# Performance work log

Measured on AMD Instinct MI355X. Metric: run time of the kernel, lower is better.

## Reference

```python
import jax, jax.numpy as jnp
import numpy as np

EPS = 1e-8  # torch.nn.CosineSimilarity default eps


def _one_sided_chamfer(ex, ey):
    # ex: [N, D], ey: [M, D]
    # cosine(ex_i, ey_j) = <ex_i, ey_j> / (max(||ex_i||, eps) * max(||ey_j||, eps))
    nx = jnp.maximum(jnp.linalg.norm(ex, axis=-1, keepdims=True), EPS)  # [N,1]
    ny = jnp.maximum(jnp.linalg.norm(ey, axis=-1, keepdims=True), EPS)  # [M,1]
    exn = ex / nx
    eyn = ey / ny
    sims = jnp.einsum('nd,md->nm', exn, eyn)  # [N, M] cosine matrix
    return jnp.max(sims, axis=-1)  # row-wise max -> [N]


def setup_inputs() -> dict:
    key = jax.random.key(0)
    k1, k2 = jax.random.split(key)
    ex = jax.random.normal(k1, (8192, 768), dtype=jnp.float32)
    ey = jax.random.normal(k2, (8192, 768), dtype=jnp.float32)
    return {"ex": ex, "ey": ey}


def reference(ex, ey):
    return _one_sided_chamfer(ex, ey)
```

## Files before the change

kernel.cpp:

```cpp
#include <hip/hip_runtime.h>
#include <math.h>

#define NROWS 8192
#define KDIM  768
#define BM 128
#define BN 128
#define BKB 128
#define KTILES (KDIM / BKB)
#define NBC 4
#define NBCG (NROWS / BN / NBC)

typedef int i32x4 __attribute__((ext_vector_type(4)));

static __device__ __forceinline__ unsigned enc_f(float f) {
    unsigned x = __float_as_uint(f);
    return (x & 0x80000000u) ? ~x : (x | 0x80000000u);
}
static __device__ __forceinline__ float dec_f(unsigned u) {
    unsigned x = (u & 0x80000000u) ? (u ^ 0x80000000u) : ~u;
    return __uint_as_float(x);
}

__global__ __launch_bounds__(256) void normalize_quant_k(
        const float* __restrict__ ex, const float* __restrict__ ey,
        signed char* __restrict__ q, float* __restrict__ scales,
        unsigned* __restrict__ out) {
    if (blockIdx.x < NROWS / 256)
        out[blockIdx.x * 256 + threadIdx.x] = enc_f(-INFINITY);
    const int wave = threadIdx.x >> 6, lane = threadIdx.x & 63;
    const int grow = blockIdx.x * 4 + wave;
    const float* src = (grow < NROWS) ? ex : ey;
    const int row = grow & (NROWS - 1);
    const float4* xr = (const float4*)(src + (size_t)row * KDIM);
    float4 v[3];
    #pragma unroll
    for (int g = 0; g < 3; ++g) v[g] = xr[lane + g * 64];
    float ss = 0.f, am = 0.f;
    #pragma unroll
    for (int g = 0; g < 3; ++g) {
        ss += v[g].x * v[g].x + v[g].y * v[g].y + v[g].z * v[g].z + v[g].w * v[g].w;
        am = fmaxf(am, fmaxf(fmaxf(fabsf(v[g].x), fabsf(v[g].y)),
                             fmaxf(fabsf(v[g].z), fabsf(v[g].w))));
    }
    #pragma unroll
    for (int off = 32; off > 0; off >>= 1) {
        ss += __shfl_xor(ss, off);
        am = fmaxf(am, __shfl_xor(am, off));
    }
    const float scale = 1.0f / fmaxf(sqrtf(ss), 1e-8f);
    am = fmaxf(am * scale, 1e-12f);
    if (lane == 0) scales[grow] = am * (1.0f / 127.0f);
    const float si = scale * (127.0f / am);
    int* dr = (int*)(q + (size_t)grow * KDIM);
    #pragma unroll
    for (int g = 0; g < 3; ++g) {
        int qx = min(127, max(-127, __float2int_rn(v[g].x * si)));
        int qy = min(127, max(-127, __float2int_rn(v[g].y * si)));
        int qz = min(127, max(-127, __float2int_rn(v[g].z * si)));
        int qw = min(127, max(-127, __float2int_rn(v[g].w * si)));
        dr[lane + g * 64] = (qx & 0xff) | ((qy & 0xff) << 8) |
                            ((qz & 0xff) << 16) | ((qw & 0xff) << 24);
    }
}

__global__ __launch_bounds__(256, 4) void gemm_rowmax_i8_k(
        const signed char* __restrict__ A, const signed char* __restrict__ B,
        const float* __restrict__ sa, const float* __restrict__ sb,
        unsigned* __restrict__ out) {
    __shared__ signed char As[BM * BKB];
    __shared__ signed char Bs[BN * BKB];

    const int tid  = threadIdx.x;
    const int wave = tid >> 6, lane = tid & 63;
    const int xcd = blockIdx.x & 7;
    const int idx = blockIdx.x >> 3;
    const int br  = (xcd >> 1) * 16 + (idx & 15);
    const int bcg = (xcd & 1) * 8 + (idx >> 4);

    const int srow   = lane >> 3;
    const int gchunk = (lane & 7) ^ srow;
    const int scol   = gchunk * 16;
    const signed char* aStage = A + (size_t)(br * BM + wave * 8 + srow) * KDIM + scol;
    signed char* lA = As + wave * 1024;
    signed char* lB = Bs + wave * 1024;

    const int wm = (wave >> 1) * 64, wn = (wave & 1) * 64;
    const int quad = lane >> 4, mrow = lane & 15;
    const int c0 = quad ^ (mrow & 7);
    const signed char* aBase = As + (wm + mrow) * BKB;
    const signed char* bBase = Bs + (wn + mrow) * BKB;
    const int row0 = br * BM + wm + quad * 4;

    #pragma unroll 1
    for (int bi = 0; bi < NBC; ++bi) {
        const int bc = bcg * NBC + bi;
        const signed char* bStage =
            B + (size_t)(bc * BN + wave * 8 + srow) * KDIM + scol;

        i32x4 acc[4][4] = {};

        #pragma unroll 1
        for (int kt = 0; kt < KTILES; ++kt) {
            __syncthreads();
            #pragma unroll
            for (int i = 0; i < 4; ++i) {
                __builtin_amdgcn_global_load_lds(
                    (const __attribute__((address_space(1))) void*)(aStage + kt * BKB + i * 24576),
                    (__attribute__((address_space(3))) void*)(lA + i * 4096), 16, 0, 0);
                __builtin_amdgcn_global_load_lds(
                    (const __attribute__((address_space(1))) void*)(bStage + kt * BKB + i * 24576),
                    (__attribute__((address_space(3))) void*)(lB + i * 4096), 16, 0, 0);
            }
            __syncthreads();

            #pragma unroll 1
            for (int ks = 0; ks < 2; ++ks) {
                const int ck = c0 ^ (ks << 2);
                i32x4 af[4], bfr[4];
                #pragma unroll
                for (int mi = 0; mi < 4; ++mi)
                    af[mi] = *(const i32x4*)(aBase + mi * 16 * BKB + ck * 16);
                #pragma unroll
                for (int ni = 0; ni < 4; ++ni)
                    bfr[ni] = *(const i32x4*)(bBase + ni * 16 * BKB + ck * 16);
                #pragma unroll
                for (int mi = 0; mi < 4; ++mi)
                    #pragma unroll
                    for (int ni = 0; ni < 4; ++ni)
                        acc[mi][ni] = __builtin_amdgcn_mfma_i32_16x16x64_i8(
                            af[mi], bfr[ni], acc[mi][ni], 0, 0, 0);
            }
        }

        float sbv[4];
        #pragma unroll
        for (int ni = 0; ni < 4; ++ni)
            sbv[ni] = sb[bc * BN + wn + ni * 16 + mrow];
        #pragma unroll
        for (int mi = 0; mi < 4; ++mi) {
            #pragma unroll
            for (int r = 0; r < 4; ++r) {
                float v = fmaxf(fmaxf((float)acc[mi][0][r] * sbv[0],
                                      (float)acc[mi][1][r] * sbv[1]),
                                fmaxf((float)acc[mi][2][r] * sbv[2],
                                      (float)acc[mi][3][r] * sbv[3]));
                v = fmaxf(v, __shfl_xor(v, 1));
                v = fmaxf(v, __shfl_xor(v, 2));
                v = fmaxf(v, __shfl_xor(v, 4));
                v = fmaxf(v, __shfl_xor(v, 8));
                if (mrow == 0) {
                    const int row = row0 + mi * 16 + r;
                    atomicMax(&out[row], enc_f(v * sa[row]));
                }
            }
        }
    }
}

__global__ void decode_out_k(unsigned* __restrict__ u) {
    int i = blockIdx.x * 256 + threadIdx.x;
    ((float*)u)[i] = dec_f(u[i]);
}

extern "C" void kernel_launch(void* const* d_in, const int* in_sizes, int n_in,
                              void* d_out, int out_size, void* d_ws, size_t ws_size,
                              hipStream_t stream) {
    (void)in_sizes; (void)n_in; (void)out_size; (void)ws_size;
    const float* ex = (const float*)d_in[0];
    const float* ey = (const float*)d_in[1];
    signed char* q = (signed char*)d_ws;
    float* scales  = (float*)(q + 2 * (size_t)NROWS * KDIM);
    unsigned* outu = (unsigned*)d_out;

    normalize_quant_k<<<(2 * NROWS) / 4, 256, 0, stream>>>(ex, ey, q, scales, outu);
    gemm_rowmax_i8_k<<<(NROWS / BM) * NBCG, 256, 0, stream>>>(
        q, q + (size_t)NROWS * KDIM, scales, scales + NROWS, outu);
    decode_out_k<<<NROWS / 256, 256, 0, stream>>>(outu);
}
```

Baseline: 156.9 us.

## Double-buffer LDS K-tiles with prefetch across column blocks in int8 GEMM

Splits the K loop into 64-byte half tiles held in two LDS buffers, so the global-to-LDS load of the next tile (continuing across column-block boundaries) is issued while MFMAs run on the current tile. The two __syncthreads per tile become one waitcnt plus barrier, the LDS layout and XOR swizzle are reworked for the new tile shape, and s_setprio raises priority around the MFMA block. This aims to hide global load latency behind compute. The cost is twice as many loop iterations and barriers, and the new swizzle may change the pattern of LDS bank conflicts.

```diff
diff --git a/kernel.cpp b/kernel.cpp
--- a/kernel.cpp
+++ b/kernel.cpp
@@ -5,9 +5,10 @@
 #define KDIM  768
 #define BM 128
 #define BN 128
-#define BKB 128
-#define KTILES (KDIM / BKB)
+#define HB 64
+#define KT2 (KDIM / HB)
 #define NBC 4
+#define NT_ALL (NBC * KT2)
 #define NBCG (NROWS / BN / NBC)
 
 typedef int i32x4 __attribute__((ext_vector_type(4)));
@@ -67,8 +68,8 @@
         const signed char* __restrict__ A, const signed char* __restrict__ B,
         const float* __restrict__ sa, const float* __restrict__ sb,
         unsigned* __restrict__ out) {
-    __shared__ signed char As[BM * BKB];
-    __shared__ signed char Bs[BN * BKB];
+    __shared__ __attribute__((aligned(128))) signed char As[2][BM * HB];
+    __shared__ __attribute__((aligned(128))) signed char Bs[2][BN * HB];
 
     const int tid  = threadIdx.x;
     const int wave = tid >> 6, lane = tid & 63;
@@ -77,61 +78,74 @@
     const int br  = (xcd >> 1) * 16 + (idx & 15);
     const int bcg = (xcd & 1) * 8 + (idx >> 4);
 
-    const int srow   = lane >> 3;
-    const int gchunk = (lane & 7) ^ srow;
-    const int scol   = gchunk * 16;
-    const signed char* aStage = A + (size_t)(br * BM + wave * 8 + srow) * KDIM + scol;
-    signed char* lA = As + wave * 1024;
-    signed char* lB = Bs + wave * 1024;
+    const int u_     = (lane & 7) ^ (lane >> 3);
+    const int srow   = ((lane >> 3) << 1) + (u_ >> 2);
+    const int gch    = (u_ & 3) * 16;
+    const signed char* aStage =
+        A + (size_t)(br * BM + wave * 32 + srow) * KDIM + gch;
+    const int ldsW = wave * 2048;
 
     const int wm = (wave >> 1) * 64, wn = (wave & 1) * 64;
     const int quad = lane >> 4, mrow = lane & 15;
-    const int c0 = quad ^ (mrow & 7);
-    const signed char* aBase = As + (wm + mrow) * BKB;
-    const signed char* bBase = Bs + (wn + mrow) * BKB;
+    const int slot = (((mrow & 1) << 2) | quad) ^ ((mrow >> 1) & 7);
+    const int aOff = ((wm >> 1) + (mrow >> 1)) * 128 + slot * 16;
+    const int bOff = ((wn >> 1) + (mrow >> 1)) * 128 + slot * 16;
     const int row0 = br * BM + wm + quad * 4;
 
+    #define GLOAD(gp, lp)                                                         \
+        __builtin_amdgcn_global_load_lds(                                         \
+            (const __attribute__((address_space(1))) void*)(gp),                  \
+            (__attribute__((address_space(3))) void*)(lp), 16, 0, 0)
+
+    #define STAGE(sidx) do {                                                      \
+        const int s_ = (sidx);                                                    \
+        const int bi_ = s_ / KT2, kt_ = s_ % KT2;                                 \
+        const signed char* ag_ = aStage + kt_ * HB;                               \
+        const signed char* bg_ = B + (size_t)((bcg * NBC + bi_) * BN              \
+                                 + wave * 32 + srow) * KDIM + gch + kt_ * HB;     \
+        signed char* la_ = &As[s_ & 1][ldsW];                                     \
+        signed char* lb_ = &Bs[s_ & 1][ldsW];                                     \
+        GLOAD(ag_, la_);  GLOAD(ag_ + 16 * KDIM, la_ + 1024);                     \
+        GLOAD(bg_, lb_);  GLOAD(bg_ + 16 * KDIM, lb_ + 1024);                     \
+    } while (0)
+
+    STAGE(0);
+    asm volatile("s_waitcnt vmcnt(0)" ::: "memory");
+    __builtin_amdgcn_s_barrier();
+
+    int t = 0;
     #pragma unroll 1
     for (int bi = 0; bi < NBC; ++bi) {
-        const int bc = bcg * NBC + bi;
-        const signed char* bStage =
-            B + (size_t)(bc * BN + wave * 8 + srow) * KDIM + scol;
+        i32x4 acc[4][4] = {};
+        #pragma unroll 1
+        for (int kt = 0; kt < KT2; ++kt, ++t) {
+            if (t + 1 < NT_ALL) STAGE(t + 1);
 
-        i32x4 acc[4][4] = {};
+            const int cb = t & 1;
+            const signed char* aP = &As[cb][aOff];
+            const signed char* bP = &Bs[cb][bOff];
+            i32x4 af[4], bfr[4];
+            #pragma unroll
+            for (int mi = 0; mi < 4; ++mi)
+                af[mi] = *(const i32x4*)(aP + mi * 1024);
+            #pragma unroll
+            for (int ni = 0; ni < 4; ++ni)
+                bfr[ni] = *(const i32x4*)(bP + ni * 1024);
 
-        #pragma unroll 1
-        for (int kt = 0; kt < KTILES; ++kt) {
-            __syncthreads();
+            __builtin_amdgcn_s_setprio(1);
             #pragma unroll
-            for (int i = 0; i < 4; ++i) {
-                __builtin_amdgcn_global_load_lds(
-                    (const __attribute__((address_space(1))) void*)(aStage + kt * BKB + i * 24576),
-                    (__attribute__((address_space(3))) void*)(lA + i * 4096), 16, 0, 0);
-                __builtin_amdgcn_global_load_lds(
-                    (const __attribute__((address_space(1))) void*)(bStage + kt * BKB + i * 24576),
-                    (__attribute__((address_space(3))) void*)(lB + i * 4096), 16, 0, 0);
-            }
-            __syncthreads();
-
-            #pragma unroll 1
-            for (int ks = 0; ks < 2; ++ks) {
-                const int ck = c0 ^ (ks << 2);
-                i32x4 af[4], bfr[4];
-                #pragma unroll
-                for (int mi = 0; mi < 4; ++mi)
-                    af[mi] = *(const i32x4*)(aBase + mi * 16 * BKB + ck * 16);
+            for (int mi = 0; mi < 4; ++mi)
                 #pragma unroll
                 for (int ni = 0; ni < 4; ++ni)
-                    bfr[ni] = *(const i32x4*)(bBase + ni * 16 * BKB + ck * 16);
-                #pragma unroll
-                for (int mi = 0; mi < 4; ++mi)
-                    #pragma unroll
-                    for (int ni = 0; ni < 4; ++ni)
-                        acc[mi][ni] = __builtin_amdgcn_mfma_i32_16x16x64_i8(
-                            af[mi], bfr[ni], acc[mi][ni], 0, 0, 0);
-            }
+                    acc[mi][ni] = __builtin_amdgcn_mfma_i32_16x16x64_i8(
+                        af[mi], bfr[ni], acc[mi][ni], 0, 0, 0);
+            __builtin_amdgcn_s_setprio(0);
+
+            asm volatile("s_waitcnt vmcnt(0)" ::: "memory");
+            __builtin_amdgcn_s_barrier();
         }
 
+        const int bc = bcg * NBC + bi;
         float sbv[4];
         #pragma unroll
         for (int ni = 0; ni < 4; ++ni)
@@ -155,6 +169,8 @@
             }
         }
     }
+    #undef STAGE
+    #undef GLOAD
 }
 
 __global__ void decode_out_k(unsigned* __restrict__ u) {
```

Measured after the change: 167.8 us. +7.0%, slower.
